# Kernel tuning notes

Hardware: AMD Instinct MI355X
Metric: run time of the kernel (lower is better)

Reference implementation:

```python
import jax, jax.numpy as jnp
import numpy as np

N, K, D = 16384, 8192, 256  # flattened tokens, codebook size, token dim


def setup_inputs() -> dict:
    key = jax.random.key(0)
    k1, k2 = jax.random.split(key)
    inputs_flatten = jax.random.normal(k1, (N, D), dtype=jnp.float32)
    embed = jax.random.normal(k2, (K, D), dtype=jnp.float32)
    return {"inputs_flatten": inputs_flatten, "embed": embed}


def reference(inputs_flatten, embed):
    x_sq = jnp.sum(inputs_flatten ** 2, axis=1, keepdims=True)          # [N, 1]
    e_sq = jnp.sum(embed ** 2, axis=1)                                  # [K]
    distances = x_sq + e_sq - 2.0 * (inputs_flatten @ embed.T)          # [N, K]
    encoding_indices = jnp.argmin(distances, axis=1)                    # [N]
    # encodings @ embed with one-hot encodings == gather rows of embed
    quantize = embed[encoding_indices]                                  # [N, D]
    # straight-through estimator
    quantize = jax.lax.stop_gradient(quantize - inputs_flatten) + inputs_flatten
    return quantize, encoding_indices[:, None]
```

## Files before the change

### kernel.cpp

```cpp
#include <hip/hip_runtime.h>
#include <float.h>
#include <limits.h>
#include <stdint.h>

constexpr int N = 16384;
constexpr int K = 8192;
constexpr int D = 256;

typedef _Float16 half8_t __attribute__((ext_vector_type(8)));
typedef float float4_t __attribute__((ext_vector_type(4)));

__global__ void vq_rowsq(const float* __restrict__ A, float* __restrict__ out) {
    int row = blockIdx.x;
    int lane = threadIdx.x;
    float4 v = ((const float4*)(A + (size_t)row * D))[lane];
    float s = v.x * v.x + v.y * v.y + v.z * v.z + v.w * v.w;
    #pragma unroll
    for (int o = 32; o > 0; o >>= 1) s += __shfl_down(s, o);
    if (lane == 0) out[row] = s;
}


__global__ void vq_prep(const float* __restrict__ X, const float* __restrict__ E,
                        _Float16* __restrict__ Xh, _Float16* __restrict__ Eh,
                        float* __restrict__ esq) {
    int c = blockIdx.x * 256 + threadIdx.x;
    const int XCH = N * 32;
    if (c < XCH) {
        int row = c >> 5, q8 = c & 31;
        int ds = q8 >> 2, q = q8 & 3;
        int rt = row >> 7, lr = row & 127;
        int slot = ((lr >> 4) << 6) + (q << 4) + (lr & 15);
        size_t dst = ((size_t)rt * 4096 + ds * 512 + slot) * 8;
        const float4* s4 = (const float4*)(X + (size_t)row * D + q8 * 8);
        float4 v0 = s4[0], v1 = s4[1];
        float x[8] = {v0.x, v0.y, v0.z, v0.w, v1.x, v1.y, v1.z, v1.w};
        half8_t hh;
        #pragma unroll
        for (int i = 0; i < 8; i++) hh[i] = (_Float16)x[i];
        *(half8_t*)(Xh + dst) = hh;
    } else {
        int cc = c - XCH;
        int code = cc >> 5, q8 = cc & 31;
        int ds = q8 >> 2, q = q8 & 3;
        int ct = code >> 7, lc = code & 127;
        int slot = ((lc >> 4) << 6) + (q << 4) + (lc & 15);
        size_t dst = ((size_t)(ct * 8 + ds) * 512 + slot) * 8;
        const float4* s4 = (const float4*)(E + (size_t)code * D + q8 * 8);
        float4 v0 = s4[0], v1 = s4[1];
        float x[8] = {v0.x, v0.y, v0.z, v0.w, v1.x, v1.y, v1.z, v1.w};
        half8_t hh;
        float sq = 0.f;
        #pragma unroll
        for (int i = 0; i < 8; i++) {
            hh[i] = (_Float16)x[i];
            sq += x[i] * x[i];
        }
        *(half8_t*)(Eh + dst) = hh;
        #pragma unroll
        for (int o = 16; o > 0; o >>= 1) sq += __shfl_xor(sq, o);
        if ((threadIdx.x & 31) == 0) esq[code] = sq;
    }
}

__device__ __forceinline__ void ldg_lds16(const _Float16* g, _Float16* l) {
    __builtin_amdgcn_global_load_lds(
        (const __attribute__((address_space(1))) unsigned int*)g,
        (__attribute__((address_space(3))) unsigned int*)l, 16, 0, 0);
}

constexpr int CS = 8;
constexpr int KT = (K / 128) / CS;
constexpr int NSTEP = KT * 8;

__global__ __launch_bounds__(256, 3) void vq_mfma(
    const _Float16* __restrict__ Xh, const _Float16* __restrict__ Eh,
    const float* __restrict__ esq, float4* __restrict__ pcand) {
    __shared__ _Float16 lds[16384];

    const int t = threadIdx.x, w = t >> 6, lane = t & 63;
    const int rt = blockIdx.x;
    const int cs = blockIdx.y;
    const int c15 = lane & 15, quad = lane >> 4;

    float best[16];
    int bidx[16];
    #pragma unroll
    for (int i = 0; i < 16; i++) { best[i] = FLT_MAX; bidx[i] = 0; }

    auto stageE = [&](int s) {
        const int ct = cs * KT + (s >> 3), ds = s & 7;
        const _Float16* src = Eh + (((size_t)ct * 8 + ds) * 512 + w * 128) * 8;
        _Float16* dst = lds + ((size_t)((s & 1) * 512 + w * 128)) * 8;
        ldg_lds16(src + (size_t)lane * 8, dst);
        ldg_lds16(src + (size_t)(64 + lane) * 8, dst + 64 * 8);
    };

    const half8_t* Xf = (const half8_t*)(Xh + (size_t)rt * 4096 * 8);
    const int arow = (w >> 1) * 256 + lane;
    half8_t Areg[2][4];
    auto loadA = [&](int ds, int par) {
        #pragma unroll
        for (int mt = 0; mt < 4; mt++)
            Areg[par][mt] = Xf[ds * 512 + arow + mt * 64];
    };

    const half8_t* C = (const half8_t*)lds;
    const int bbase = (w & 1) * 256 + lane;

    float4_t acc[4][4];
    #pragma unroll
    for (int mt = 0; mt < 4; mt++)
        #pragma unroll
        for (int nt = 0; nt < 4; nt++) acc[mt][nt] = {0.f, 0.f, 0.f, 0.f};

    loadA(0, 0);
    stageE(0);

    #pragma unroll 2
    for (int s = 0; s < NSTEP; s++) {
        __syncthreads();
        if (s + 1 < NSTEP) {
            stageE(s + 1);
            loadA((s + 1) & 7, (s + 1) & 1);
        }

        const int b = (s & 1) * 512;
        half8_t B[4];
        #pragma unroll
        for (int nt = 0; nt < 4; nt++) B[nt] = C[b + bbase + nt * 64];

        #pragma unroll
        for (int mt = 0; mt < 4; mt++)
            #pragma unroll
            for (int nt = 0; nt < 4; nt++)
                acc[mt][nt] = __builtin_amdgcn_mfma_f32_16x16x32_f16(
                    Areg[s & 1][mt], B[nt], acc[mt][nt], 0, 0, 0);

        if ((s & 7) == 7) {
            const int code0 = (cs * KT + (s >> 3)) * 128 + (w & 1) * 64;
            #pragma unroll
            for (int nt = 0; nt < 4; nt++) {
                const int code = code0 + nt * 16 + c15;
                const float eq = esq[code];
                #pragma unroll
                for (int mt = 0; mt < 4; mt++)
                    #pragma unroll
                    for (int rg = 0; rg < 4; rg++) {
                        float sc = fmaf(-2.f, acc[mt][nt][rg], eq);
                        int sl = mt * 4 + rg;
                        if (sc < best[sl]) { best[sl] = sc; bidx[sl] = code; }
                    }
            }
            #pragma unroll
            for (int mt = 0; mt < 4; mt++)
                #pragma unroll
                for (int nt = 0; nt < 4; nt++) acc[mt][nt] = {0.f, 0.f, 0.f, 0.f};
        }
    }

    __syncthreads();
    float* smin = (float*)lds;
    int* sidx = (int*)lds + 4096;
    const int cont = (w & 1) * 16 + c15;
    #pragma unroll
    for (int sl = 0; sl < 16; sl++) {
        int row = (w >> 1) * 64 + (sl >> 2) * 16 + quad * 4 + (sl & 3);
        smin[cont * 128 + row] = best[sl];
        sidx[cont * 128 + row] = bidx[sl];
    }
    __syncthreads();
    if (t < 128) {
        float m1 = FLT_MAX, m2 = FLT_MAX;
        int i1 = 0, i2 = 0;
        for (int c = 0; c < 32; c++) {
            float v = smin[c * 128 + t];
            int id = sidx[c * 128 + t];
            if (v < m1 || (v == m1 && id < i1)) {
                m2 = m1; i2 = i1; m1 = v; i1 = id;
            } else if (v < m2 || (v == m2 && id < i2)) {
                m2 = v; i2 = id;
            }
        }
        uint32_t pk = ((uint32_t)i1 << 13) | (uint32_t)(i2 & 8191);
        float4 out;
        out.x = m1; out.y = m2; out.z = __int_as_float((int)pk); out.w = 0.f;
        pcand[(size_t)(rt * 128 + t) * CS + cs] = out;
    }
}

__device__ __forceinline__ float wave_sum(float v) {
    #pragma unroll
    for (int o = 1; o < 64; o <<= 1) v += __shfl_xor(v, o);
    return v;
}

__global__ void vq_rescore(const float* __restrict__ X, const float* __restrict__ E,
                           const float4* __restrict__ pcand, float* __restrict__ out_q,
                           float* __restrict__ out_idx) {
    constexpr float EB = 0.4f;
    int row = blockIdx.x * 4 + (threadIdx.x >> 6);
    int lane = threadIdx.x & 63;

    int cand[2 * CS];
    float csc[2 * CS];
    float gm1 = FLT_MAX, gm2 = FLT_MAX;
    int gi1 = INT_MAX;
    #pragma unroll
    for (int s = 0; s < CS; s++) {
        float4 p = pcand[(size_t)row * CS + s];
        uint32_t pk = (uint32_t)__float_as_int(p.z);
        int i1 = (int)(pk >> 13), i2 = (int)(pk & 8191);
        cand[2 * s] = i1;
        csc[2 * s] = p.x;
        cand[2 * s + 1] = i2;
        csc[2 * s + 1] = p.y;
        if (p.x < gm1 || (p.x == gm1 && i1 < gi1)) {
            gm2 = gm1; gm1 = p.x; gi1 = i1;
        } else if (p.x < gm2) gm2 = p.x;
        if (p.y < gm2) gm2 = p.y;
    }

    int besti = gi1;
    if (gm2 - gm1 <= EB) {
        float4 xv = ((const float4*)(X + (size_t)row * D))[lane];
        float xs = wave_sum(xv.x * xv.x + xv.y * xv.y + xv.z * xv.z + xv.w * xv.w);
        float bestv = FLT_MAX;
        besti = INT_MAX;
        for (int c = 0; c < 2 * CS; c++) {
            if (csc[c] > gm1 + EB) continue;
            int idx = cand[c];
            float4 e = ((const float4*)(E + (size_t)idx * D))[lane];
            float dp = wave_sum(xv.x * e.x + xv.y * e.y + xv.z * e.z + xv.w * e.w);
            float eq = wave_sum(e.x * e.x + e.y * e.y + e.z * e.z + e.w * e.w);
            float sc = (xs + eq) - 2.f * dp;
            if (sc < bestv || (sc == bestv && idx < besti)) { bestv = sc; besti = idx; }
        }
    }
    if (lane == 0) out_idx[row] = (float)besti;
    float4 bv = ((const float4*)(E + (size_t)besti * D))[lane];
    ((float4*)(out_q + (size_t)row * D))[lane] = bv;
}

constexpr int BM = 128, BN = 128, DK = 32, KSPLIT = 8;
constexpr int KCHUNK = K / KSPLIT;
constexpr int LDX = BM + 4, LDE = BN + 4;

__global__ __launch_bounds__(256) void vq_main(
    const float* __restrict__ X, const float* __restrict__ E,
    const float* __restrict__ xsq, const float* __restrict__ esq,
    float* __restrict__ pmin, int* __restrict__ pidx) {
    __shared__ float sx[DK * LDX];
    __shared__ float se[DK * LDE];
    const int t = threadIdx.x;
    const int row0 = blockIdx.x * BM;
    const int kbeg = blockIdx.y * KCHUNK;
    const int lane = t & 63, wave = t >> 6;
    const int lm = lane >> 3, ln = lane & 7;
    const int mf = (wave >> 1) * 64 + lm * 8;
    const int nf = (wave & 1) * 64 + ln * 8;
    float xs[8];
    #pragma unroll
    for (int i = 0; i < 8; i++) xs[i] = xsq[row0 + mf + i];
    float rmin[8];
    int ridx[8];
    #pragma unroll
    for (int i = 0; i < 8; i++) { rmin[i] = FLT_MAX; ridx[i] = 0; }
    const int sm = t >> 3;
    const int sd = (t & 7) * 4;
    for (int kt = kbeg; kt < kbeg + KCHUNK; kt += BN) {
        float acc[8][8];
        #pragma unroll
        for (int i = 0; i < 8; i++)
            #pragma unroll
            for (int j = 0; j < 8; j++) acc[i][j] = 0.0f;
        for (int d0 = 0; d0 < D; d0 += DK) {
            __syncthreads();
            #pragma unroll
            for (int r = 0; r < 4; r++) {
                int row = sm + 32 * r;
                float4 v = *(const float4*)(X + (size_t)(row0 + row) * D + d0 + sd);
                sx[(sd + 0) * LDX + row] = v.x;
                sx[(sd + 1) * LDX + row] = v.y;
                sx[(sd + 2) * LDX + row] = v.z;
                sx[(sd + 3) * LDX + row] = v.w;
                float4 ww = *(const float4*)(E + (size_t)(kt + row) * D + d0 + sd);
                se[(sd + 0) * LDE + row] = ww.x;
                se[(sd + 1) * LDE + row] = ww.y;
                se[(sd + 2) * LDE + row] = ww.z;
                se[(sd + 3) * LDE + row] = ww.w;
            }
            __syncthreads();
            #pragma unroll
            for (int d = 0; d < DK; d++) {
                float4 a0 = *(const float4*)(sx + d * LDX + mf);
                float4 a1 = *(const float4*)(sx + d * LDX + mf + 4);
                float4 b0 = *(const float4*)(se + d * LDE + nf);
                float4 b1 = *(const float4*)(se + d * LDE + nf + 4);
                float a[8] = {a0.x, a0.y, a0.z, a0.w, a1.x, a1.y, a1.z, a1.w};
                float b[8] = {b0.x, b0.y, b0.z, b0.w, b1.x, b1.y, b1.z, b1.w};
                #pragma unroll
                for (int i = 0; i < 8; i++)
                    #pragma unroll
                    for (int j = 0; j < 8; j++) acc[i][j] += a[i] * b[j];
            }
        }
        float es[8];
        #pragma unroll
        for (int j = 0; j < 8; j++) es[j] = esq[kt + nf + j];
        #pragma unroll
        for (int i = 0; i < 8; i++)
            #pragma unroll
            for (int j = 0; j < 8; j++) {
                float s = (xs[i] + es[j]) - 2.0f * acc[i][j];
                if (s < rmin[i]) { rmin[i] = s; ridx[i] = kt + nf + j; }
            }
    }
    __syncthreads();
    float* redm = sx;
    int* redi = (int*)se;
    const int c = (wave & 1) * 8 + ln;
    #pragma unroll
    for (int i = 0; i < 8; i++) {
        int r = (wave >> 1) * 64 + lm * 8 + i;
        redm[r * 16 + c] = rmin[i];
        redi[r * 16 + c] = ridx[i];
    }
    __syncthreads();
    if (t < BM) {
        float bst = redm[t * 16];
        int bi = redi[t * 16];
        #pragma unroll
        for (int c2 = 1; c2 < 16; c2++) {
            float v = redm[t * 16 + c2];
            int id = redi[t * 16 + c2];
            if (v < bst || (v == bst && id < bi)) { bst = v; bi = id; }
        }
        pmin[(size_t)(row0 + t) * KSPLIT + blockIdx.y] = bst;
        pidx[(size_t)(row0 + t) * KSPLIT + blockIdx.y] = bi;
    }
}

__global__ void vq_final(const float* __restrict__ E, const float* __restrict__ pmin,
                         const int* __restrict__ pidx, float* __restrict__ out_q,
                         float* __restrict__ out_idx) {
    int row = blockIdx.x;
    int lane = threadIdx.x;
    float bst = pmin[(size_t)row * KSPLIT];
    int bi = pidx[(size_t)row * KSPLIT];
    #pragma unroll
    for (int s = 1; s < KSPLIT; s++) {
        float v = pmin[(size_t)row * KSPLIT + s];
        int id = pidx[(size_t)row * KSPLIT + s];
        if (v < bst || (v == bst && id < bi)) { bst = v; bi = id; }
    }
    if (lane == 0) out_idx[row] = (float)bi;
    float4 v = ((const float4*)(E + (size_t)bi * D))[lane];
    ((float4*)(out_q + (size_t)row * D))[lane] = v;
}

extern "C" void kernel_launch(void* const* d_in, const int* in_sizes, int n_in,
                              void* d_out, int out_size, void* d_ws, size_t ws_size,
                              hipStream_t stream) {
    const float* X = (const float*)d_in[0];
    const float* E = (const float*)d_in[1];
    float* out_q = (float*)d_out;
    float* out_idx = (float*)d_out + (size_t)N * D;

    const size_t need = (size_t)12 * 1024 * 1024 + 32768 + (size_t)N * CS * 16;
    if (ws_size >= need) {
        _Float16* Xh = (_Float16*)d_ws;
        _Float16* Eh = Xh + (size_t)N * D;
        float* esq = (float*)(Eh + (size_t)K * D);
        float4* pcand = (float4*)(esq + K);

        vq_prep<<<(N + K) * 32 / 256, 256, 0, stream>>>(X, E, Xh, Eh, esq);
        dim3 grid(N / 128, CS);
        vq_mfma<<<grid, 256, 0, stream>>>(Xh, Eh, esq, pcand);
        vq_rescore<<<N / 4, 256, 0, stream>>>(X, E, pcand, out_q, out_idx);
    } else {
        float* esq = (float*)d_ws;
        float* xsq = esq + K;
        float* pmin = xsq + N;
        int* pidx = (int*)(pmin + (size_t)N * KSPLIT);
        vq_rowsq<<<K, 64, 0, stream>>>(E, esq);
        vq_rowsq<<<N, 64, 0, stream>>>(X, xsq);
        dim3 grid(N / BM, KSPLIT);
        vq_main<<<grid, 256, 0, stream>>>(X, E, xsq, esq, pmin, pidx);
        vq_final<<<N, 64, 0, stream>>>(E, pmin, pidx, out_q, out_idx);
    }
}
```

Baseline: 176.1 us.

## Keep X tile resident in LDS and stream codebook from global into registers

The whole 128-row X tile (all 256 dims) is loaded into LDS once at kernel start, and codebook fragments are instead double-buffered directly from global memory into registers each step. This removes the per-step __syncthreads and the async E staging into LDS. The trade-off is twice the LDS footprint, so launch bounds drop from 3 to 2 blocks per CU, and B loads now come straight from global or L2 with no LDS sharing between waves.

```diff
diff --git a/kernel.cpp b/kernel.cpp
--- a/kernel.cpp
+++ b/kernel.cpp
@@ -73,10 +73,10 @@
 constexpr int KT = (K / 128) / CS;
 constexpr int NSTEP = KT * 8;
 
-__global__ __launch_bounds__(256, 3) void vq_mfma(
+__global__ __launch_bounds__(256, 2) void vq_mfma(
     const _Float16* __restrict__ Xh, const _Float16* __restrict__ Eh,
     const float* __restrict__ esq, float4* __restrict__ pcand) {
-    __shared__ _Float16 lds[16384];
+    __shared__ _Float16 lds[32768];
 
     const int t = threadIdx.x, w = t >> 6, lane = t & 63;
     const int rt = blockIdx.x;
@@ -88,54 +88,50 @@
     #pragma unroll
     for (int i = 0; i < 16; i++) { best[i] = FLT_MAX; bidx[i] = 0; }
 
-    auto stageE = [&](int s) {
-        const int ct = cs * KT + (s >> 3), ds = s & 7;
-        const _Float16* src = Eh + (((size_t)ct * 8 + ds) * 512 + w * 128) * 8;
-        _Float16* dst = lds + ((size_t)((s & 1) * 512 + w * 128)) * 8;
-        ldg_lds16(src + (size_t)lane * 8, dst);
-        ldg_lds16(src + (size_t)(64 + lane) * 8, dst + 64 * 8);
+    {
+        const _Float16* src = Xh + ((size_t)rt * 4096 + w * 1024) * 8;
+        _Float16* dst = lds + (size_t)(w * 1024) * 8;
+        #pragma unroll
+        for (int i = 0; i < 16; i++)
+            ldg_lds16(src + (size_t)(i * 64 + lane) * 8, dst + i * 512);
+    }
+
+    const half8_t* C = (const half8_t*)lds;
+    const int abase = (w >> 1) * 256 + lane;
+    const half8_t* Bf = (const half8_t*)Eh;
+    const int bbase = (w & 1) * 256 + lane;
+
+    float4_t acc[4][4];
+    #pragma unroll
+    for (int mt = 0; mt < 4; mt++)
+        #pragma unroll
+        for (int nt = 0; nt < 4; nt++) acc[mt][nt] = {0.f, 0.f, 0.f, 0.f};
+
+    half8_t Breg[2][4];
+    auto loadB = [&](int s, int par) {
+        const size_t rbase = (size_t)(cs * KT * 8 + s) * 512 + bbase;
+        #pragma unroll
+        for (int nt = 0; nt < 4; nt++) Breg[par][nt] = Bf[rbase + nt * 64];
     };
 
-    const half8_t* Xf = (const half8_t*)(Xh + (size_t)rt * 4096 * 8);
-    const int arow = (w >> 1) * 256 + lane;
-    half8_t Areg[2][4];
-    auto loadA = [&](int ds, int par) {
-        #pragma unroll
-        for (int mt = 0; mt < 4; mt++)
-            Areg[par][mt] = Xf[ds * 512 + arow + mt * 64];
-    };
-
-    const half8_t* C = (const half8_t*)lds;
-    const int bbase = (w & 1) * 256 + lane;
-
-    float4_t acc[4][4];
-    #pragma unroll
-    for (int mt = 0; mt < 4; mt++)
-        #pragma unroll
-        for (int nt = 0; nt < 4; nt++) acc[mt][nt] = {0.f, 0.f, 0.f, 0.f};
-
-    loadA(0, 0);
-    stageE(0);
+    loadB(0, 0);
+    __syncthreads();
 
     #pragma unroll 2
     for (int s = 0; s < NSTEP; s++) {
-        __syncthreads();
-        if (s + 1 < NSTEP) {
-            stageE(s + 1);
-            loadA((s + 1) & 7, (s + 1) & 1);
-        }
-
-        const int b = (s & 1) * 512;
-        half8_t B[4];
-        #pragma unroll
-        for (int nt = 0; nt < 4; nt++) B[nt] = C[b + bbase + nt * 64];
+        if (s + 1 < NSTEP) loadB(s + 1, (s + 1) & 1);
+
+        const int ds = s & 7;
+        half8_t A[4];
+        #pragma unroll
+        for (int mt = 0; mt < 4; mt++) A[mt] = C[ds * 512 + abase + mt * 64];
 
         #pragma unroll
         for (int mt = 0; mt < 4; mt++)
             #pragma unroll
             for (int nt = 0; nt < 4; nt++)
                 acc[mt][nt] = __builtin_amdgcn_mfma_f32_16x16x32_f16(
-                    Areg[s & 1][mt], B[nt], acc[mt][nt], 0, 0, 0);
+                    A[mt], Breg[s & 1][nt], acc[mt][nt], 0, 0, 0);
 
         if ((s & 7) == 7) {
             const int code0 = (cs * KT + (s >> 3)) * 128 + (w & 1) * 64;
```

Result: faster. 162.0 us (-8.0%).
